# Optimization experiments

Hardware: AMD Instinct MI355X
Metric: run time of the kernel (lower is better)

## Reference

```python
import jax, jax.numpy as jnp
import numpy as np

B, S, HID, NH = 8, 384, 512, 8
HD = HID // NH
SCALE = float(np.sqrt(HID))  # torch code scales by sqrt(full hidden_units), not head dim
EPS = 1e-6


def setup_inputs() -> dict:
    key = jax.random.key(0)
    ks = jax.random.split(key, 6)
    enc = jax.random.normal(ks[0], (B, S, HID), jnp.float32)
    # mask: (B,1,S,S); fill=ones, made causal (lower-triangular) so masking is exercised
    mask = jnp.broadcast_to(jnp.tril(jnp.ones((S, S), jnp.int32)), (B, 1, S, S))
    init = 1.0 / np.sqrt(HID)
    Wq = jax.random.normal(ks[1], (HID, HID), jnp.float32) * init
    Wk = jax.random.normal(ks[2], (HID, HID), jnp.float32) * init
    Wv = jax.random.normal(ks[3], (HID, HID), jnp.float32) * init
    Wo = jax.random.normal(ks[4], (HID, HID), jnp.float32) * init
    ln_gamma = jnp.ones((HID,), jnp.float32)
    ln_beta = jnp.zeros((HID,), jnp.float32)
    return {"enc": enc, "mask": mask, "Wq": Wq, "Wk": Wk, "Wv": Wv, "Wo": Wo,
            "ln_gamma": ln_gamma, "ln_beta": ln_beta}


def reference(enc, mask, Wq, Wk, Wv, Wo, ln_gamma, ln_beta):
    # enc: (B,S,HID); torch Linear(no bias): y = x @ W.T
    def heads(x, W):
        return (x @ W.T).reshape(B, S, NH, HD).transpose(0, 2, 1, 3)  # (B,H,S,D)

    q, k, v = heads(enc, Wq), heads(enc, Wk), heads(enc, Wv)
    # intersample scores: query (b,h,q) vs key (c,h,k) -> (B,H,C,Sq,Sk)
    scores = jnp.einsum('bhqd,chkd->bhcqk', q, k) / SCALE
    m = mask[:, 0]  # (C,S,S): key-sample mask
    scores = jnp.where(m[None, None] == 0, -1.0e9, scores)
    # joint softmax over (key-sample c, key-position k)
    sw = scores.transpose(0, 1, 3, 2, 4).reshape(B, NH, S, B * S)
    w = jax.nn.softmax(sw, axis=-1).reshape(B, NH, S, B, S).transpose(0, 1, 3, 2, 4)  # (B,H,C,Sq,Sk)
    ctx = jnp.einsum('bhcqk,chkd->bhqd', w, v)            # (B,H,S,D)
    ctx = ctx.transpose(0, 2, 1, 3).reshape(B, S, HID)     # (B,S,HID)
    out = ctx @ Wo.T + enc                                 # W_O + residual (dropout=identity, eval)
    mu = out.mean(-1, keepdims=True)
    var = ((out - mu) ** 2).mean(-1, keepdims=True)
    out = (out - mu) / jnp.sqrt(var + EPS) * ln_gamma + ln_beta
    return (out, w)
```

## Files before the change

### kernel.cpp

```cpp
#include <hip/hip_runtime.h>
#include <hip/hip_bf16.h>

#define B_    8
#define S_    384
#define HID_  512
#define NH_   8
#define HD_   64
#define T_    3072
static constexpr float INV_SCALE = 0.044194173824159216f;

typedef float  f32x4  __attribute__((ext_vector_type(4)));
typedef __bf16 bf16x8 __attribute__((ext_vector_type(8)));
typedef __bf16 bf16x4 __attribute__((ext_vector_type(4)));

#define MFMA(a, b, c) __builtin_amdgcn_mfma_f32_16x16x32_bf16((a), (b), (c), 0, 0, 0)

__global__ __launch_bounds__(256)
void cvt_kernel(const float* __restrict__ enc, const float* __restrict__ Wq,
                const float* __restrict__ Wk,  const float* __restrict__ Wv,
                const float* __restrict__ Wo,
                __bf16* __restrict__ encB, __bf16* __restrict__ WqB,
                __bf16* __restrict__ WkB,  __bf16* __restrict__ WvB,
                __bf16* __restrict__ WoB)
{
    const int E  = T_ * HID_ / 4;
    const int W4 = HID_ * HID_ / 4;
    int i = blockIdx.x * 256 + threadIdx.x;
    const float* src; __bf16* dst; int off;
    if      (i < E)          { src = enc; dst = encB; off = i; }
    else if (i < E + W4)     { src = Wq;  dst = WqB;  off = i - E; }
    else if (i < E + 2 * W4) { src = Wk;  dst = WkB;  off = i - E - W4; }
    else if (i < E + 3 * W4) { src = Wv;  dst = WvB;  off = i - E - 2 * W4; }
    else                     { src = Wo;  dst = WoB;  off = i - E - 3 * W4; }
    f32x4 v = *(const f32x4*)(src + (size_t)off * 4);
    bf16x4 o;
    #pragma unroll
    for (int j = 0; j < 4; ++j) o[j] = (__bf16)v[j];
    *(bf16x4*)(dst + (size_t)off * 4) = o;
}

__global__ __launch_bounds__(256)
void qkv_kernel(const __bf16* __restrict__ enc,
                const __bf16* __restrict__ Wq,
                const __bf16* __restrict__ Wk,
                const __bf16* __restrict__ Wv,
                __bf16* __restrict__ Qs,
                __bf16* __restrict__ Ks,
                __bf16* __restrict__ Vt)
{
    const int w    = threadIdx.x >> 6;
    const int lane = threadIdx.x & 63;
    const int col  = lane & 15;
    const int quad = lane >> 4;
    const int m0   = blockIdx.x * 64 + w * 16;
    const int n0   = blockIdx.y * 64;
    const int z    = blockIdx.z;
    const __bf16* W = (z == 0) ? Wq : (z == 1) ? Wk : Wv;

    f32x4 acc[4];
    #pragma unroll
    for (int j = 0; j < 4; ++j) acc[j] = (f32x4){0.f, 0.f, 0.f, 0.f};

    const __bf16* arow = enc + (size_t)(m0 + col) * HID_;
    for (int k0 = 0; k0 < HID_; k0 += 32) {
        bf16x8 a = *(const bf16x8*)(arow + k0 + quad * 8);
        #pragma unroll
        for (int j = 0; j < 4; ++j) {
            bf16x8 b = *(const bf16x8*)(W + (size_t)(n0 + j * 16 + col) * HID_ + k0 + quad * 8);
            acc[j] = MFMA(a, b, acc[j]);
        }
    }

    if (z == 2) {
        #pragma unroll
        for (int j = 0; j < 4; ++j) {
            int n = n0 + j * 16 + col;
            bf16x4 pk;
            #pragma unroll
            for (int r = 0; r < 4; ++r) pk[r] = (__bf16)acc[j][r];
            *(bf16x4*)(Vt + (size_t)n * T_ + m0 + quad * 4) = pk;
        }
    } else {
        __bf16* Oo = (z == 0) ? Qs : Ks;
        float sc = (z == 0) ? INV_SCALE : 1.0f;
        #pragma unroll
        for (int j = 0; j < 4; ++j)
            #pragma unroll
            for (int r = 0; r < 4; ++r)
                Oo[(size_t)(m0 + quad * 4 + r) * HID_ + n0 + j * 16 + col] =
                    (__bf16)(acc[j][r] * sc);
    }
}

__global__ __launch_bounds__(256)
void attn_kernel(const __bf16* __restrict__ Qs,
                 const __bf16* __restrict__ Ks,
                 const __bf16* __restrict__ Vt,
                 float* __restrict__ wout,
                 __bf16* __restrict__ ctxB)
{
    const int qt   = blockIdx.x;
    const int h    = blockIdx.y;
    const int b    = blockIdx.z;
    const int tid  = threadIdx.x;
    const int w    = tid >> 6;
    const int lane = tid & 63;
    const int col  = lane & 15;
    const int quad = lane >> 4;

    __shared__ __bf16 elds[4][16][72];
    __shared__ float  rl_lds[64];

    const int qq_base = w * 16 + quad * 4;

    const __bf16* qrow = Qs + (size_t)(b * S_ + qt * 64 + w * 16 + col) * HID_ + h * HD_;
    bf16x8 aQ0 = *(const bf16x8*)(qrow + quad * 8);
    bf16x8 aQ1 = *(const bf16x8*)(qrow + 32 + quad * 8);

    f32x4 acc[4];
    #pragma unroll
    for (int j = 0; j < 4; ++j) acc[j] = (f32x4){0.f, 0.f, 0.f, 0.f};
    float lp[4] = {0.f, 0.f, 0.f, 0.f};

    for (int c = 0; c < B_; ++c) {
        for (int kc = 0; kc <= qt; ++kc) {
            const int kt0 = c * S_ + kc * 64;
            const bool diag = (kc == qt);
            #pragma unroll
            for (int nt = 0; nt < 4; ++nt) {
                const __bf16* krow = Ks + (size_t)(kt0 + nt * 16 + col) * HID_ + h * HD_;
                bf16x8 bK0 = *(const bf16x8*)(krow + quad * 8);
                bf16x8 bK1 = *(const bf16x8*)(krow + 32 + quad * 8);
                f32x4 s = (f32x4){0.f, 0.f, 0.f, 0.f};
                s = MFMA(aQ0, bK0, s);
                s = MFMA(aQ1, bK1, s);
                const int kk = nt * 16 + col;
                #pragma unroll
                for (int r = 0; r < 4; ++r) {
                    float e = (!diag || kk <= qq_base + r) ? __expf(s[r]) : 0.f;
                    lp[r] += e;
                    elds[w][quad * 4 + r][kk] = (__bf16)e;
                    size_t widx = ((((size_t)(b * NH_ + h) * B_ + c) * S_ +
                                    (qt * 64 + qq_base + r)) * S_ + kc * 64 + kk);
                    wout[widx] = e;
                }
            }
            #pragma unroll
            for (int ks = 0; ks < 2; ++ks) {
                bf16x8 aE = *(const bf16x8*)(&elds[w][col][ks * 32 + quad * 8]);
                #pragma unroll
                for (int nt = 0; nt < 4; ++nt) {
                    bf16x8 bV = *(const bf16x8*)(Vt + (size_t)(h * HD_ + nt * 16 + col) * T_ +
                                                 kt0 + ks * 32 + quad * 8);
                    acc[nt] = MFMA(aE, bV, acc[nt]);
                }
            }
        }
    }

    float rl[4];
    #pragma unroll
    for (int r = 0; r < 4; ++r) {
        float v = lp[r];
        v += __shfl_xor(v, 1);
        v += __shfl_xor(v, 2);
        v += __shfl_xor(v, 4);
        v += __shfl_xor(v, 8);
        rl[r] = 1.0f / v;
    }
    if (col == 0) {
        #pragma unroll
        for (int r = 0; r < 4; ++r) rl_lds[qq_base + r] = rl[r];
    }

    #pragma unroll
    for (int nt = 0; nt < 4; ++nt)
        #pragma unroll
        for (int r = 0; r < 4; ++r)
            ctxB[(size_t)(b * S_ + qt * 64 + qq_base + r) * HID_ + h * HD_ + nt * 16 + col] =
                (__bf16)(acc[nt][r] * rl[r]);

    __syncthreads();

    const int kmax = (qt + 1) * 64;
    float* wblk = wout + (size_t)(b * NH_ + h) * B_ * S_ * S_;
    for (int idx = tid; idx < 512 * 96; idx += 256) {
        int row = idx / 96, c4 = idx - row * 96;
        int c = row >> 6, qp = row & 63;
        int k0 = c4 * 4;
        float* p = wblk + ((size_t)c * S_ + qt * 64 + qp) * S_ + k0;
        if (k0 >= kmax) {
            *(f32x4*)p = (f32x4){0.f, 0.f, 0.f, 0.f};
        } else {
            float rlv = rl_lds[qp];
            f32x4 v = *(const f32x4*)p;
            #pragma unroll
            for (int j = 0; j < 4; ++j) v[j] *= rlv;
            *(f32x4*)p = v;
        }
    }
}

__global__ __launch_bounds__(256)
void out_kernel(const __bf16* __restrict__ ctxB,
                const __bf16* __restrict__ WoB,
                const float* __restrict__ enc,
                const float* __restrict__ gamma,
                const float* __restrict__ beta,
                float* __restrict__ out)
{
    const int t0   = blockIdx.x * 32;
    const int tid  = threadIdx.x;
    const int w    = tid >> 6;
    const int lane = tid & 63;
    const int col  = lane & 15;
    const int quad = lane >> 4;
    const int tg   = w >> 1;
    const int half = w & 1;

    __shared__ float s_sums[2][16][2][2];

    f32x4 acc[16];
    #pragma unroll
    for (int nt = 0; nt < 16; ++nt) acc[nt] = (f32x4){0.f, 0.f, 0.f, 0.f};

    const __bf16* arow = ctxB + (size_t)(t0 + tg * 16 + col) * HID_;
    for (int step = 0; step < 16; ++step) {
        bf16x8 a = *(const bf16x8*)(arow + step * 32 + quad * 8);
        #pragma unroll
        for (int nt = 0; nt < 16; ++nt) {
            bf16x8 bW = *(const bf16x8*)(WoB + (size_t)(half * 256 + nt * 16 + col) * HID_ +
                                         step * 32 + quad * 8);
            acc[nt] = MFMA(a, bW, acc[nt]);
        }
    }

    const int trow = t0 + tg * 16 + quad * 4;
    float psum[4] = {0.f, 0.f, 0.f, 0.f};
    float psq[4]  = {0.f, 0.f, 0.f, 0.f};
    #pragma unroll
    for (int nt = 0; nt < 16; ++nt) {
        int n = half * 256 + nt * 16 + col;
        #pragma unroll
        for (int r = 0; r < 4; ++r) {
            float x = acc[nt][r] + enc[(size_t)(trow + r) * HID_ + n];
            acc[nt][r] = x;
            psum[r] += x;
            psq[r]  += x * x;
        }
    }
    #pragma unroll
    for (int r = 0; r < 4; ++r) {
        float v = psum[r], q2 = psq[r];
        v  += __shfl_xor(v, 1);  v  += __shfl_xor(v, 2);
        v  += __shfl_xor(v, 4);  v  += __shfl_xor(v, 8);
        q2 += __shfl_xor(q2, 1); q2 += __shfl_xor(q2, 2);
        q2 += __shfl_xor(q2, 4); q2 += __shfl_xor(q2, 8);
        if (col == 0) {
            s_sums[tg][quad * 4 + r][half][0] = v;
            s_sums[tg][quad * 4 + r][half][1] = q2;
        }
    }
    __syncthreads();

    #pragma unroll
    for (int r = 0; r < 4; ++r) {
        float sm = s_sums[tg][quad * 4 + r][0][0] + s_sums[tg][quad * 4 + r][1][0];
        float sq = s_sums[tg][quad * 4 + r][0][1] + s_sums[tg][quad * 4 + r][1][1];
        float mu   = sm * (1.0f / 512.0f);
        float var  = sq * (1.0f / 512.0f) - mu * mu;
        float rstd = rsqrtf(var + 1e-6f);
        #pragma unroll
        for (int nt = 0; nt < 16; ++nt) {
            int n = half * 256 + nt * 16 + col;
            float y = (acc[nt][r] - mu) * rstd * gamma[n] + beta[n];
            out[(size_t)(trow + r) * HID_ + n] = y;
        }
    }
}

extern "C" void kernel_launch(void* const* d_in, const int* in_sizes, int n_in,
                              void* d_out, int out_size, void* d_ws, size_t ws_size,
                              hipStream_t stream)
{
    const float* enc   = (const float*)d_in[0];
    const float* Wq    = (const float*)d_in[2];
    const float* Wk    = (const float*)d_in[3];
    const float* Wv    = (const float*)d_in[4];
    const float* Wo    = (const float*)d_in[5];
    const float* gamma = (const float*)d_in[6];
    const float* beta  = (const float*)d_in[7];

    float* out  = (float*)d_out;
    float* wout = out + (size_t)T_ * HID_;

    char* ws = (char*)d_ws;
    const size_t SZ_TOK = (size_t)T_ * HID_ * sizeof(__bf16);
    const size_t SZ_W   = (size_t)HID_ * HID_ * sizeof(__bf16);
    __bf16* encB = (__bf16*)(ws);
    __bf16* WqB  = (__bf16*)(ws + SZ_TOK);
    __bf16* WkB  = (__bf16*)(ws + SZ_TOK + SZ_W);
    __bf16* WvB  = (__bf16*)(ws + SZ_TOK + 2 * SZ_W);
    __bf16* WoB  = (__bf16*)(ws + SZ_TOK + 3 * SZ_W);
    __bf16* Qs   = (__bf16*)(ws + SZ_TOK + 4 * SZ_W);
    __bf16* Ks   = (__bf16*)(ws + 2 * SZ_TOK + 4 * SZ_W);
    __bf16* Vt   = (__bf16*)(ws + 3 * SZ_TOK + 4 * SZ_W);
    __bf16* ctxB = (__bf16*)(ws + 4 * SZ_TOK + 4 * SZ_W);

    cvt_kernel<<<dim3(2560), 256, 0, stream>>>(enc, Wq, Wk, Wv, Wo,
                                               encB, WqB, WkB, WvB, WoB);
    qkv_kernel<<<dim3(48, 8, 3), 256, 0, stream>>>(encB, WqB, WkB, WvB, Qs, Ks, Vt);
    attn_kernel<<<dim3(6, NH_, B_), 256, 0, stream>>>(Qs, Ks, Vt, wout, ctxB);
    out_kernel<<<dim3(96), 256, 0, stream>>>(ctxB, WoB, enc, gamma, beta, out);
}
```

Measured before the change: 671.1 us.

## Split attention-weight output into separate recompute kernel and halve out_kernel tile

The attention kernel no longer writes unnormalized weights and then rereads and rescales them. It now stores only per-row reciprocal sums to workspace. A new w_writer kernel with 8x more blocks recomputes QK^T exp, scales it and writes the normalized weight tensor once, with coalesced stores staged through LDS, and zero-fills the masked tiles. This removes the read-modify-write pass over the large weight output and improves parallelism, at the cost of recomputing the scores. The output projection kernel also uses 16-row tiles over 192 blocks instead of 32-row tiles over 96. rlws aliases the encB workspace, which is already consumed by then.

```diff
diff --git a/kernel.cpp b/kernel.cpp
--- a/kernel.cpp
+++ b/kernel.cpp
@@ -93,11 +93,11 @@
 }
 
 __global__ __launch_bounds__(256)
-void attn_kernel(const __bf16* __restrict__ Qs,
-                 const __bf16* __restrict__ Ks,
-                 const __bf16* __restrict__ Vt,
-                 float* __restrict__ wout,
-                 __bf16* __restrict__ ctxB)
+void attn_core(const __bf16* __restrict__ Qs,
+               const __bf16* __restrict__ Ks,
+               const __bf16* __restrict__ Vt,
+               __bf16* __restrict__ ctxB,
+               float* __restrict__ rlws)
 {
     const int qt   = blockIdx.x;
     const int h    = blockIdx.y;
@@ -109,7 +109,6 @@
     const int quad = lane >> 4;
 
     __shared__ __bf16 elds[4][16][72];
-    __shared__ float  rl_lds[64];
 
     const int qq_base = w * 16 + quad * 4;
 
@@ -140,9 +139,6 @@
                     float e = (!diag || kk <= qq_base + r) ? __expf(s[r]) : 0.f;
                     lp[r] += e;
                     elds[w][quad * 4 + r][kk] = (__bf16)e;
-                    size_t widx = ((((size_t)(b * NH_ + h) * B_ + c) * S_ +
-                                    (qt * 64 + qq_base + r)) * S_ + kc * 64 + kk);
-                    wout[widx] = e;
                 }
             }
             #pragma unroll
@@ -170,7 +166,8 @@
     }
     if (col == 0) {
         #pragma unroll
-        for (int r = 0; r < 4; ++r) rl_lds[qq_base + r] = rl[r];
+        for (int r = 0; r < 4; ++r)
+            rlws[(size_t)(b * NH_ + h) * S_ + qt * 64 + qq_base + r] = rl[r];
     }
 
     #pragma unroll
@@ -179,25 +176,70 @@
         for (int r = 0; r < 4; ++r)
             ctxB[(size_t)(b * S_ + qt * 64 + qq_base + r) * HID_ + h * HD_ + nt * 16 + col] =
                 (__bf16)(acc[nt][r] * rl[r]);
-
-    __syncthreads();
-
-    const int kmax = (qt + 1) * 64;
-    float* wblk = wout + (size_t)(b * NH_ + h) * B_ * S_ * S_;
-    for (int idx = tid; idx < 512 * 96; idx += 256) {
-        int row = idx / 96, c4 = idx - row * 96;
-        int c = row >> 6, qp = row & 63;
-        int k0 = c4 * 4;
-        float* p = wblk + ((size_t)c * S_ + qt * 64 + qp) * S_ + k0;
-        if (k0 >= kmax) {
-            *(f32x4*)p = (f32x4){0.f, 0.f, 0.f, 0.f};
-        } else {
-            float rlv = rl_lds[qp];
-            f32x4 v = *(const f32x4*)p;
-            #pragma unroll
-            for (int j = 0; j < 4; ++j) v[j] *= rlv;
-            *(f32x4*)p = v;
-        }
+}
+
+__global__ __launch_bounds__(256)
+void w_writer(const __bf16* __restrict__ Qs,
+              const __bf16* __restrict__ Ks,
+              const float* __restrict__ rlws,
+              float* __restrict__ wout)
+{
+    const int x    = blockIdx.x;
+    const int qt   = x % 6;
+    const int c    = x / 6;
+    const int h    = blockIdx.y;
+    const int b    = blockIdx.z;
+    const int tid  = threadIdx.x;
+    const int w    = tid >> 6;
+    const int lane = tid & 63;
+    const int col  = lane & 15;
+    const int quad = lane >> 4;
+    const int wr   = lane >> 2;
+    const int seg  = lane & 3;
+
+    __shared__ float elds[4][16][68];
+
+    const int qq_base = w * 16 + quad * 4;
+
+    const __bf16* qrow = Qs + (size_t)(b * S_ + qt * 64 + w * 16 + col) * HID_ + h * HD_;
+    bf16x8 aQ0 = *(const bf16x8*)(qrow + quad * 8);
+    bf16x8 aQ1 = *(const bf16x8*)(qrow + 32 + quad * 8);
+
+    float rlv[4];
+    #pragma unroll
+    for (int r = 0; r < 4; ++r)
+        rlv[r] = rlws[(size_t)(b * NH_ + h) * S_ + qt * 64 + qq_base + r];
+
+    float* gb = wout + ((((size_t)(b * NH_ + h) * B_ + c) * S_ + qt * 64 + w * 16 + wr) * S_);
+
+    for (int kc = 0; kc < 6; ++kc) {
+        float* gp = gb + kc * 64 + seg * 16;
+        if (kc > qt) {
+            #pragma unroll
+            for (int j = 0; j < 4; ++j)
+                *(f32x4*)(gp + j * 4) = (f32x4){0.f, 0.f, 0.f, 0.f};
+            continue;
+        }
+        const int kt0 = c * S_ + kc * 64;
+        const bool diag = (kc == qt);
+        #pragma unroll
+        for (int nt = 0; nt < 4; ++nt) {
+            const __bf16* krow = Ks + (size_t)(kt0 + nt * 16 + col) * HID_ + h * HD_;
+            bf16x8 bK0 = *(const bf16x8*)(krow + quad * 8);
+            bf16x8 bK1 = *(const bf16x8*)(krow + 32 + quad * 8);
+            f32x4 s = (f32x4){0.f, 0.f, 0.f, 0.f};
+            s = MFMA(aQ0, bK0, s);
+            s = MFMA(aQ1, bK1, s);
+            const int kk = nt * 16 + col;
+            #pragma unroll
+            for (int r = 0; r < 4; ++r) {
+                float e = (!diag || kk <= qq_base + r) ? __expf(s[r]) * rlv[r] : 0.f;
+                elds[w][quad * 4 + r][kk] = e;
+            }
+        }
+        #pragma unroll
+        for (int j = 0; j < 4; ++j)
+            *(f32x4*)(gp + j * 4) = *(const f32x4*)(&elds[w][wr][seg * 16 + j * 4]);
     }
 }
 
@@ -209,38 +251,36 @@
                 const float* __restrict__ beta,
                 float* __restrict__ out)
 {
-    const int t0   = blockIdx.x * 32;
+    const int t0   = blockIdx.x * 16;
     const int tid  = threadIdx.x;
-    const int w    = tid >> 6;
+    const int wv   = tid >> 6;
     const int lane = tid & 63;
     const int col  = lane & 15;
     const int quad = lane >> 4;
-    const int tg   = w >> 1;
-    const int half = w & 1;
-
-    __shared__ float s_sums[2][16][2][2];
-
-    f32x4 acc[16];
-    #pragma unroll
-    for (int nt = 0; nt < 16; ++nt) acc[nt] = (f32x4){0.f, 0.f, 0.f, 0.f};
-
-    const __bf16* arow = ctxB + (size_t)(t0 + tg * 16 + col) * HID_;
+
+    __shared__ float s_sums[16][4][2];
+
+    f32x4 acc[8];
+    #pragma unroll
+    for (int nt = 0; nt < 8; ++nt) acc[nt] = (f32x4){0.f, 0.f, 0.f, 0.f};
+
+    const __bf16* arow = ctxB + (size_t)(t0 + col) * HID_;
     for (int step = 0; step < 16; ++step) {
         bf16x8 a = *(const bf16x8*)(arow + step * 32 + quad * 8);
         #pragma unroll
-        for (int nt = 0; nt < 16; ++nt) {
-            bf16x8 bW = *(const bf16x8*)(WoB + (size_t)(half * 256 + nt * 16 + col) * HID_ +
+        for (int nt = 0; nt < 8; ++nt) {
+            bf16x8 bW = *(const bf16x8*)(WoB + (size_t)(wv * 128 + nt * 16 + col) * HID_ +
                                          step * 32 + quad * 8);
             acc[nt] = MFMA(a, bW, acc[nt]);
         }
     }
 
-    const int trow = t0 + tg * 16 + quad * 4;
+    const int trow = t0 + quad * 4;
     float psum[4] = {0.f, 0.f, 0.f, 0.f};
     float psq[4]  = {0.f, 0.f, 0.f, 0.f};
     #pragma unroll
-    for (int nt = 0; nt < 16; ++nt) {
-        int n = half * 256 + nt * 16 + col;
+    for (int nt = 0; nt < 8; ++nt) {
+        int n = wv * 128 + nt * 16 + col;
         #pragma unroll
         for (int r = 0; r < 4; ++r) {
             float x = acc[nt][r] + enc[(size_t)(trow + r) * HID_ + n];
@@ -257,22 +297,24 @@
         q2 += __shfl_xor(q2, 1); q2 += __shfl_xor(q2, 2);
         q2 += __shfl_xor(q2, 4); q2 += __shfl_xor(q2, 8);
         if (col == 0) {
-            s_sums[tg][quad * 4 + r][half][0] = v;
-            s_sums[tg][quad * 4 + r][half][1] = q2;
+            s_sums[quad * 4 + r][wv][0] = v;
+            s_sums[quad * 4 + r][wv][1] = q2;
         }
     }
     __syncthreads();
 
     #pragma unroll
     for (int r = 0; r < 4; ++r) {
-        float sm = s_sums[tg][quad * 4 + r][0][0] + s_sums[tg][quad * 4 + r][1][0];
-        float sq = s_sums[tg][quad * 4 + r][0][1] + s_sums[tg][quad * 4 + r][1][1];
+        float sm = s_sums[quad * 4 + r][0][0] + s_sums[quad * 4 + r][1][0] +
+                   s_sums[quad * 4 + r][2][0] + s_sums[quad * 4 + r][3][0];
+        float sq = s_sums[quad * 4 + r][0][1] + s_sums[quad * 4 + r][1][1] +
+                   s_sums[quad * 4 + r][2][1] + s_sums[quad * 4 + r][3][1];
         float mu   = sm * (1.0f / 512.0f);
         float var  = sq * (1.0f / 512.0f) - mu * mu;
         float rstd = rsqrtf(var + 1e-6f);
         #pragma unroll
-        for (int nt = 0; nt < 16; ++nt) {
-            int n = half * 256 + nt * 16 + col;
+        for (int nt = 0; nt < 8; ++nt) {
+            int n = wv * 128 + nt * 16 + col;
             float y = (acc[nt][r] - mu) * rstd * gamma[n] + beta[n];
             out[(size_t)(trow + r) * HID_ + n] = y;
         }
@@ -306,10 +348,12 @@
     __bf16* Ks   = (__bf16*)(ws + 2 * SZ_TOK + 4 * SZ_W);
     __bf16* Vt   = (__bf16*)(ws + 3 * SZ_TOK + 4 * SZ_W);
     __bf16* ctxB = (__bf16*)(ws + 4 * SZ_TOK + 4 * SZ_W);
+    float*  rlws = (float*)(ws);
 
     cvt_kernel<<<dim3(2560), 256, 0, stream>>>(enc, Wq, Wk, Wv, Wo,
                                                encB, WqB, WkB, WvB, WoB);
     qkv_kernel<<<dim3(48, 8, 3), 256, 0, stream>>>(encB, WqB, WkB, WvB, Qs, Ks, Vt);
-    attn_kernel<<<dim3(6, NH_, B_), 256, 0, stream>>>(Qs, Ks, Vt, wout, ctxB);
-    out_kernel<<<dim3(96), 256, 0, stream>>>(ctxB, WoB, enc, gamma, beta, out);
-}
+    attn_core<<<dim3(6, NH_, B_), 256, 0, stream>>>(Qs, Ks, Vt, ctxB, rlws);
+    w_writer<<<dim3(48, NH_, B_), 256, 0, stream>>>(Qs, Ks, rlws, wout);
+    out_kernel<<<dim3(192), 256, 0, stream>>>(ctxB, WoB, enc, gamma, beta, out);
+}
```

New measurement: 622.7 us. 1.08x faster.
